# Performance work log

Measured on AMD Instinct MI355X. Metric: run time of the kernel, lower is better.

Reference implementation:

```python
import math
import jax, jax.numpy as jnp
import numpy as np

# ---- DeepSeek-V2-Lite decoder layer config ----
H = 16            # num_attention_heads
D_NOPE = 128      # qk_nope_head_dim
D_ROPE = 64       # qk_rope_head_dim
D_Q = D_NOPE + D_ROPE  # q_head_dim = 192
D_V = 128         # v_head_dim
KV_RANK = 512     # kv_lora_rank
HID = 2048        # hidden_size
INTER = 10944     # intermediate_size (dense MLP)
MAX_POS = 8192
BASE = 10000.0
FACTOR = 40.0     # yarn scaling factor
ORIG_MAX = 4096
BETA_FAST, BETA_SLOW = 32, 1
MSCALE = 0.707
MSCALE_ALL = 0.707
EPS = 1e-6


def _yarn_cos_sin():
    # DeepseekV2LiteYarnRotaryEmbedding._set_cos_sin_cache
    dim = D_ROPE
    ar = np.arange(0, dim, 2, dtype=np.float32) / dim
    freq_extra = 1.0 / BASE ** ar
    freq_inter = 1.0 / (FACTOR * BASE ** ar)

    def corr_dim(num_rot):
        return dim * math.log(ORIG_MAX / (num_rot * 2 * math.pi)) / (2 * math.log(BASE))

    low = max(math.floor(corr_dim(BETA_FAST)), 0)
    high = min(math.ceil(corr_dim(BETA_SLOW)), dim - 1)
    hi = high + 0.001 if low == high else high
    ramp = np.clip((np.arange(dim // 2, dtype=np.float32) - low) / (hi - low), 0.0, 1.0)
    inv_freq_mask = 1.0 - ramp
    inv_freq = freq_inter * (1 - inv_freq_mask) + freq_extra * inv_freq_mask
    t = np.arange(MAX_POS, dtype=np.float32)
    freqs = np.outer(t, inv_freq)

    def get_mscale(s, m):
        return 1.0 if s <= 1 else 0.1 * m * math.log(s) + 1.0

    ms = get_mscale(FACTOR, MSCALE) / get_mscale(FACTOR, MSCALE_ALL)
    emb = np.concatenate([freqs, freqs], axis=-1)
    return jnp.asarray(np.cos(emb) * ms, jnp.float32), jnp.asarray(np.sin(emb) * ms, jnp.float32)

COS_CACHE, SIN_CACHE = _yarn_cos_sin()  # [MAX_POS, D_ROPE]


def _rms(x, w):
    return x * jax.lax.rsqrt(jnp.mean(x * x, axis=-1, keepdims=True) + EPS) * w


def _deinterleave(x):
    # view(..., d//2, 2).transpose(-1, -2).reshape(..., d)
    d = x.shape[-1]
    return x.reshape(x.shape[:-1] + (d // 2, 2)).swapaxes(-1, -2).reshape(x.shape)


def _apply_rope(x, cos, sin):
    x = _deinterleave(x)
    d = x.shape[-1]
    x1, x2 = x[..., : d // 2], x[..., d // 2:]
    return x * cos + jnp.concatenate([-x2, x1], axis=-1) * sin


def _decoder_layer(hidden_states, position_ids, Wq, Wkva, w_kvln, Wkvb, Wo, Wg, Wu, Wd, w_ln1, w_ln2):
    b, s, _ = hidden_states.shape
    dt = hidden_states.dtype

    # ---- attention block ----
    residual = hidden_states
    x = _rms(hidden_states, w_ln1)

    q = (x @ Wq.T).reshape(b, s, H, D_Q)                 # [b,s,h,192]
    q_nope, q_pe = q[..., :D_NOPE], q[..., D_NOPE:]

    ckv = x @ Wkva.T                                     # [b,s,576]
    c, k_pe = ckv[..., :KV_RANK], ckv[..., KV_RANK:][:, :, None, :]  # [b,s,512],[b,s,1,64]
    kv = (_rms(c, w_kvln) @ Wkvb.T).reshape(b, s, H, D_NOPE + D_V)
    k_nope, v = kv[..., :D_NOPE], kv[..., D_NOPE:]

    cos = COS_CACHE[position_ids][:, :, None, :].astype(dt)  # unsqueeze_dim=2
    sin = SIN_CACHE[position_ids][:, :, None, :].astype(dt)
    q_pe = _apply_rope(q_pe, cos, sin)
    k_pe = _apply_rope(k_pe, cos, sin)

    qf = jnp.concatenate([q_nope, q_pe], axis=-1)                          # [b,s,h,192]
    kf = jnp.concatenate([k_nope, jnp.broadcast_to(k_pe, (b, s, H, D_ROPE))], axis=-1)

    scale = D_Q ** -0.5
    scores = jnp.einsum('bqhd,bkhd->bhqk', qf, kf) * scale
    causal = jnp.tril(jnp.ones((s, s), dtype=bool))
    scores = jnp.where(causal, scores, jnp.finfo(scores.dtype).min)
    probs = jax.nn.softmax(scores, axis=-1)
    attn = jnp.einsum('bhqk,bkhd->bqhd', probs, v).reshape(b, s, H * D_V)
    x = residual + attn @ Wo.T

    # ---- MLP block (SwiGLU) ----
    residual = x
    y = _rms(x, w_ln2)
    x = residual + (jax.nn.silu(y @ Wg.T) * (y @ Wu.T)) @ Wd.T
    return x


def setup_inputs() -> dict:
    key = jax.random.key(0)
    ks = jax.random.split(key, 12)
    B, S = 2, 2048
    sd = 0.02
    inp = {
        'hidden_states': jax.random.normal(ks[0], (B, S, HID), jnp.float32),
        'position_ids': jnp.broadcast_to(jnp.arange(S, dtype=jnp.int32), (B, S)),
        'Wq': jax.random.normal(ks[1], (H * D_Q, HID), jnp.float32) * sd,
        'Wkva': jax.random.normal(ks[2], (KV_RANK + D_ROPE, HID), jnp.float32) * sd,
        'w_kvln': jnp.ones((KV_RANK,), jnp.float32),
        'Wkvb': jax.random.normal(ks[3], (H * (D_NOPE + D_V), KV_RANK), jnp.float32) * sd,
        'Wo': jax.random.normal(ks[4], (HID, H * D_V), jnp.float32) * sd,
        'Wg': jax.random.normal(ks[5], (INTER, HID), jnp.float32) * sd,
        'Wu': jax.random.normal(ks[6], (INTER, HID), jnp.float32) * sd,
        'Wd': jax.random.normal(ks[7], (HID, INTER), jnp.float32) * sd,
        'w_ln1': jnp.ones((HID,), jnp.float32),
        'w_ln2': jnp.ones((HID,), jnp.float32),
    }
    return inp


def reference(hidden_states, position_ids, Wq, Wkva, w_kvln, Wkvb, Wo, Wg, Wu, Wd, w_ln1, w_ln2):
    return _decoder_layer(hidden_states, position_ids, Wq, Wkva, w_kvln, Wkvb, Wo, Wg, Wu, Wd, w_ln1, w_ln2)
```

## Files before the change

kernel.cpp:

```cpp
#include <hip/hip_runtime.h>
#include <hip/hip_bf16.h>
#include <math.h>


typedef short short8 __attribute__((ext_vector_type(8)));
typedef short short4v __attribute__((ext_vector_type(4)));
typedef float f32x4 __attribute__((ext_vector_type(4)));

static __device__ __forceinline__ float bf2f(ushort u) {
  union { uint i; float f; } v; v.i = ((uint)u) << 16; return v.f;
}
static __device__ __forceinline__ ushort f2bf(float x) {
  union { float f; uint i; } v; v.f = x;
  uint r = v.i + 0x7fffu + ((v.i >> 16) & 1u);
  return (ushort)(r >> 16);
}

static __device__ __forceinline__ void glds16(const ushort* g, ushort* l) {
  __builtin_amdgcn_global_load_lds(
      (const __attribute__((address_space(1))) unsigned int*)g,
      (__attribute__((address_space(3))) unsigned int*)l, 16, 0, 0);
}

__global__ __launch_bounds__(256)
void cvt_bf16(const float* __restrict__ in, ushort* __restrict__ out, int n8) {
  int i = blockIdx.x * 256 + threadIdx.x;
  if (i >= n8) return;
  float4 a = ((const float4*)in)[2 * i];
  float4 b = ((const float4*)in)[2 * i + 1];
  short8 o;
  o[0] = (short)f2bf(a.x); o[1] = (short)f2bf(a.y);
  o[2] = (short)f2bf(a.z); o[3] = (short)f2bf(a.w);
  o[4] = (short)f2bf(b.x); o[5] = (short)f2bf(b.y);
  o[6] = (short)f2bf(b.z); o[7] = (short)f2bf(b.w);
  ((short8*)out)[i] = o;
}

__global__ __launch_bounds__(256)
void rms_bf16(const float* __restrict__ in, int istride, int width, float inv_w,
              const float* __restrict__ w, ushort* __restrict__ out, int ostride) {
  const int row = blockIdx.x;
  const float* x = in + (size_t)row * istride;
  float ss = 0.f;
  for (int i = threadIdx.x; i < width; i += 256) { float v = x[i]; ss += v * v; }
#pragma unroll
  for (int off = 32; off > 0; off >>= 1) ss += __shfl_xor(ss, off);
  __shared__ float red[4];
  if ((threadIdx.x & 63) == 0) red[threadIdx.x >> 6] = ss;
  __syncthreads();
  float tot = red[0] + red[1] + red[2] + red[3];
  float scale = rsqrtf(tot * inv_w + 1e-6f);
  ushort* o = out + (size_t)row * ostride;
  for (int i = threadIdx.x; i < width; i += 256) o[i] = f2bf(x[i] * scale * w[i]);
}

template<int EPI>
__global__ __launch_bounds__(256, 2)
void gemm_as(const ushort* __restrict__ A, const ushort* __restrict__ B,
             void* __restrict__ Cv, const void* __restrict__ resv,
             int M, int N, int K) {
  __shared__ ushort As[128 * 64];
  __shared__ ushort Bs[128 * 64];
  const int tid = threadIdx.x;
  const int wave = tid >> 6, lane = tid & 63;
  const int m0 = blockIdx.x * 128, n0 = blockIdx.y * 128;
  const int lm = lane & 15, quad = lane >> 4;
  const int wm = (wave & 1) * 64, wn = (wave >> 1) * 64;

  const int lrow = lane >> 3;
  const int lcq  = lane & 7;
  const int gu   = lcq ^ lrow;
  const ushort* gA[4];
  const ushort* gB[4];
  ushort* lA[4];
  ushort* lB[4];
#pragma unroll
  for (int j = 0; j < 4; ++j) {
    const int r = wave * 32 + j * 8 + lrow;
    gA[j] = A + (size_t)(m0 + r) * K + gu * 8;
    int br = n0 + r; if (br > N - 1) br = N - 1;
    gB[j] = B + (size_t)br * K + gu * 8;
    lA[j] = &As[(wave * 32 + j * 8) * 64];
    lB[j] = &Bs[(wave * 32 + j * 8) * 64];
  }

  f32x4 acc[4][4];
  const f32x4 z4 = {0.f, 0.f, 0.f, 0.f};
#pragma unroll
  for (int i = 0; i < 4; ++i)
#pragma unroll
    for (int j = 0; j < 4; ++j) acc[i][j] = z4;

  const int sw = lm & 7;

  for (int k0 = 0; k0 < K; k0 += 64) {
#pragma unroll
    for (int j = 0; j < 4; ++j) glds16(gA[j] + k0, lA[j]);
#pragma unroll
    for (int j = 0; j < 4; ++j) glds16(gB[j] + k0, lB[j]);
    __syncthreads();

#pragma unroll
    for (int kk = 0; kk < 2; ++kk) {
      const int us = ((kk * 4 + quad) ^ sw) * 8;
      short8 afr[4], bfr[4];
#pragma unroll
      for (int mt = 0; mt < 4; ++mt)
        afr[mt] = *(const short8*)&As[(wm + mt * 16 + lm) * 64 + us];
#pragma unroll
      for (int nt = 0; nt < 4; ++nt)
        bfr[nt] = *(const short8*)&Bs[(wn + nt * 16 + lm) * 64 + us];
#pragma unroll
      for (int mt = 0; mt < 4; ++mt)
#pragma unroll
        for (int nt = 0; nt < 4; ++nt)
          acc[mt][nt] = __builtin_amdgcn_mfma_f32_16x16x32_bf16(
              afr[mt], bfr[nt], acc[mt][nt], 0, 0, 0);
    }
    __syncthreads();
  }

#pragma unroll
  for (int mt = 0; mt < 4; ++mt) {
#pragma unroll
    for (int r = 0; r < 4; ++r) {
      const int grow = m0 + wm + mt * 16 + quad * 4 + r;
#pragma unroll
      for (int nt = 0; nt < 4; ++nt) {
        const int gcol = n0 + wn + nt * 16 + lm;
        if (gcol < N) {
          const size_t idx = (size_t)grow * N + gcol;
          float vacc = acc[mt][nt][r];
          if (EPI == 0) {
            ((ushort*)Cv)[idx] = f2bf(vacc);
          } else if (EPI == 1) {
            ((float*)Cv)[idx] = vacc;
          } else if (EPI == 2) {
            ((float*)Cv)[idx] = vacc + ((const float*)resv)[idx];
          } else if (EPI == 3) {
            float gv = bf2f(((const ushort*)resv)[idx]);
            ((ushort*)Cv)[idx] = f2bf(gv / (1.f + __expf(-gv)) * vacc);
          } else {
            if (gcol < 3072)
              ((ushort*)Cv)[(size_t)grow * 3072 + gcol] = f2bf(vacc);
            else
              ((float*)resv)[(size_t)grow * 576 + (gcol - 3072)] = vacc;
          }
        }
      }
    }
  }
}

__global__ __launch_bounds__(64)
void rope_kernel(ushort* __restrict__ q, const float* __restrict__ ckv,
                 const int* __restrict__ pos_ids, ushort* __restrict__ kpe) {
  const int t = blockIdx.x;
  const int j = threadIdx.x;
  const int j2 = j & 31;
  const float ar = (float)j2 * (1.f / 32.f);
  const float fe = exp2f(-ar * 13.287712379549449f);
  const float fi = fe * 0.025f;
  float ramp = ((float)j2 - 10.f) * (1.f / 13.f);
  ramp = fminf(fmaxf(ramp, 0.f), 1.f);
  const float invf = fi * ramp + fe * (1.f - ramp);
  const float ang = (float)pos_ids[t] * invf;
  float s, c;
  __sincosf(ang, &s, &c);
  const bool lo = j < 32;
  {
    const float* kp = ckv + (size_t)t * 576 + 512;
    float x0 = kp[2 * j2], x1 = kp[2 * j2 + 1];
    float o = lo ? (x0 * c - x1 * s) : (x1 * c + x0 * s);
    kpe[(size_t)t * 64 + j] = f2bf(o);
  }
  for (int h = 0; h < 16; ++h) {
    ushort* qp = q + (size_t)t * 3072 + h * 192 + 128;
    float x0 = bf2f(qp[2 * j2]), x1 = bf2f(qp[2 * j2 + 1]);
    float o = lo ? (x0 * c - x1 * s) : (x1 * c + x0 * s);
    __syncthreads();
    qp[j] = f2bf(o);
  }
}

__global__ __launch_bounds__(256, 2)
void attn_mfma(const ushort* __restrict__ q, const ushort* __restrict__ kv,
               const ushort* __restrict__ kpe, ushort* __restrict__ out) {
  const int qt = (int)gridDim.x - 1 - (int)blockIdx.x;
  const int bh = blockIdx.y;
  const int b = bh >> 4, h = bh & 15;
  const int tid = threadIdx.x;
  const int wave = tid >> 6, lane = tid & 63;
  const int lm = lane & 15, quad = lane >> 4;
  const int wq = wave * 32;
  const float scale = 0.07216878364870323f;

  __shared__ __align__(16) char smem[62464];
  ushort (*Ks)[200] = (ushort(*)[200])smem;
  ushort (*Vt)[72]  = (ushort(*)[72])(smem + 25600);
  ushort (*Pm)[72]  = (ushort(*)[72])(smem + 44032);
  ushort (*Qs)[200] = (ushort(*)[200])smem;

  const size_t tok0 = (size_t)b * 2048;
  const int q0 = qt * 128;

  {
    const ushort* qbase = q + (tok0 + q0) * 3072 + (size_t)h * 192;
#pragma unroll
    for (int it = 0; it < 12; ++it) {
      int idx = (it * 256 + tid) * 8;
      int row = idx / 192, col = idx % 192;
      *(uint4*)&Qs[row][col] = *(const uint4*)(qbase + (size_t)row * 3072 + col);
    }
  }
  __syncthreads();
  short8 qf[2][6];
#pragma unroll
  for (int mt = 0; mt < 2; ++mt)
#pragma unroll
    for (int kk = 0; kk < 6; ++kk)
      qf[mt][kk] = *(const short8*)&Qs[wq + mt * 16 + lm][kk * 32 + quad * 8];
  __syncthreads();

  f32x4 o[2][8];
  const f32x4 z4 = {0.f, 0.f, 0.f, 0.f};
#pragma unroll
  for (int mt = 0; mt < 2; ++mt)
#pragma unroll
    for (int nt = 0; nt < 8; ++nt) o[mt][nt] = z4;
  float m_run[8], l_run[8];
#pragma unroll
  for (int i = 0; i < 8; ++i) { m_run[i] = -3.0e38f; l_run[i] = 0.f; }

  const int nkt = 2 * qt + 2;
  for (int kt = 0; kt < nkt; ++kt) {
    const int kb = kt * 64;
    {
      const int krow = tid >> 2, kq = tid & 3;
      const ushort* src = kv + ((tok0 + kb + krow) * 16 + h) * 256 + kq * 32;
#pragma unroll
      for (int i = 0; i < 4; ++i)
        *(uint4*)&Ks[krow][kq * 32 + i * 8] = *(const uint4*)(src + i * 8);
      const ushort* psrc = kpe + (tok0 + kb + krow) * 64 + kq * 16;
      *(uint4*)&Ks[krow][128 + kq * 16]     = *(const uint4*)(psrc);
      *(uint4*)&Ks[krow][128 + kq * 16 + 8] = *(const uint4*)(psrc + 8);
      const int kgrp = (tid & 15) * 4, dgrp = (tid >> 4) * 8;
      uint4 vv[4];
#pragma unroll
      for (int i = 0; i < 4; ++i)
        vv[i] = *(const uint4*)(kv + ((tok0 + kb + kgrp + i) * 16 + h) * 256 + 128 + dgrp);
#pragma unroll
      for (int j = 0; j < 8; ++j) {
        short4v w;
#pragma unroll
        for (int i = 0; i < 4; ++i) w[i] = (short)((const ushort*)&vv[i])[j];
        *(short4v*)&Vt[dgrp + j][kgrp] = w;
      }
    }
    __syncthreads();

    f32x4 s_acc[2][4];
#pragma unroll
    for (int mt = 0; mt < 2; ++mt)
#pragma unroll
      for (int nt = 0; nt < 4; ++nt) s_acc[mt][nt] = z4;
#pragma unroll
    for (int kk = 0; kk < 6; ++kk) {
      short8 kf[4];
#pragma unroll
      for (int nt = 0; nt < 4; ++nt)
        kf[nt] = *(const short8*)&Ks[nt * 16 + lm][kk * 32 + quad * 8];
#pragma unroll
      for (int mt = 0; mt < 2; ++mt)
#pragma unroll
        for (int nt = 0; nt < 4; ++nt)
          s_acc[mt][nt] = __builtin_amdgcn_mfma_f32_16x16x32_bf16(
              qf[mt][kk], kf[nt], s_acc[mt][nt], 0, 0, 0);
    }

    const bool full = (kb + 63) <= (q0 + wq);
#pragma unroll
    for (int mt = 0; mt < 2; ++mt) {
#pragma unroll
      for (int r = 0; r < 4; ++r) {
        const int qg = q0 + wq + mt * 16 + quad * 4 + r;
        float sv[4];
        float rm = -3.0e38f;
        if (full) {
#pragma unroll
          for (int nt = 0; nt < 4; ++nt) {
            float s = s_acc[mt][nt][r] * scale;
            sv[nt] = s;
            rm = fmaxf(rm, s);
          }
        } else {
#pragma unroll
          for (int nt = 0; nt < 4; ++nt) {
            const int key = kb + nt * 16 + lm;
            float s = s_acc[mt][nt][r] * scale;
            s = (key <= qg) ? s : -3.0e38f;
            sv[nt] = s;
            rm = fmaxf(rm, s);
          }
        }
#pragma unroll
        for (int off = 1; off < 16; off <<= 1) rm = fmaxf(rm, __shfl_xor(rm, off));
        const int li = mt * 4 + r;
        const float mnew = fmaxf(m_run[li], rm);
        const float alpha = __expf(m_run[li] - mnew);
        m_run[li] = mnew;
        float rs = 0.f;
        ushort pb[4];
#pragma unroll
        for (int nt = 0; nt < 4; ++nt) {
          float p = __expf(sv[nt] - mnew);
          rs += p;
          pb[nt] = f2bf(p);
        }
#pragma unroll
        for (int off = 1; off < 16; off <<= 1) rs += __shfl_xor(rs, off);
        l_run[li] = l_run[li] * alpha + rs;
#pragma unroll
        for (int nt = 0; nt < 8; ++nt) o[mt][nt][r] *= alpha;
        const int qrow = wq + mt * 16 + quad * 4 + r;
#pragma unroll
        for (int nt = 0; nt < 4; ++nt) Pm[qrow][nt * 16 + lm] = pb[nt];
      }
    }

#pragma unroll
    for (int kt2 = 0; kt2 < 2; ++kt2) {
      short8 pa[2];
#pragma unroll
      for (int mt = 0; mt < 2; ++mt)
        pa[mt] = *(const short8*)&Pm[wq + mt * 16 + lm][kt2 * 32 + quad * 8];
#pragma unroll
      for (int nt = 0; nt < 8; ++nt) {
        short8 vb = *(const short8*)&Vt[nt * 16 + lm][kt2 * 32 + quad * 8];
#pragma unroll
        for (int mt = 0; mt < 2; ++mt)
          o[mt][nt] = __builtin_amdgcn_mfma_f32_16x16x32_bf16(
              pa[mt], vb, o[mt][nt], 0, 0, 0);
      }
    }
    __syncthreads();
  }

  ushort* obase = out + (tok0 + q0) * 2048 + h * 128;
#pragma unroll
  for (int mt = 0; mt < 2; ++mt) {
#pragma unroll
    for (int r = 0; r < 4; ++r) {
      const int qrow = wq + mt * 16 + quad * 4 + r;
      const float inv = 1.f / l_run[mt * 4 + r];
#pragma unroll
      for (int nt = 0; nt < 8; ++nt)
        obase[(size_t)qrow * 2048 + nt * 16 + lm] = f2bf(o[mt][nt][r] * inv);
    }
  }
}

extern "C" void kernel_launch(void* const* d_in, const int* in_sizes, int n_in,
                              void* d_out, int out_size, void* d_ws, size_t ws_size,
                              hipStream_t stream) {
  const float* hidden = (const float*)d_in[0];
  const int*   pos    = (const int*)d_in[1];
  const float* Wq     = (const float*)d_in[2];
  const float* Wkva   = (const float*)d_in[3];
  const float* w_kvln = (const float*)d_in[4];
  const float* Wkvb   = (const float*)d_in[5];
  const float* Wo     = (const float*)d_in[6];
  const float* Wg     = (const float*)d_in[7];
  const float* Wu     = (const float*)d_in[8];
  const float* Wd     = (const float*)d_in[9];
  const float* w_ln1  = (const float*)d_in[10];
  const float* w_ln2  = (const float*)d_in[11];
  float* out = (float*)d_out;

  char* ws = (char*)d_ws;
  ushort* xn    = (ushort*)(ws);
  char*   R1    = ws + 16777216;
  ushort* qb    = (ushort*)(R1);
  float*  ckv   = (float*)(R1 + 25165824);
  ushort* cn    = (ushort*)(R1 + 34603008);
  ushort* kvb   = (ushort*)(R1 + 38797312);
  ushort* kpe   = (ushort*)(R1 + 72351744);
  ushort* attno = (ushort*)(R1 + 72876032);
  ushort* gb    = (ushort*)(R1);
  float*  h1    = (float*)(ws + 196083712);

  char* WSL = ws + 106430464;
  ushort* wq_bf   = (ushort*)(WSL);
  ushort* wkva_bf = (ushort*)(WSL + 12582912);
  ushort* wkvb_bf = (ushort*)(WSL + 14942208);
  ushort* wo_bf   = (ushort*)(WSL + 19136512);
  ushort* wg_bf   = (ushort*)(WSL);
  ushort* wu_bf   = (ushort*)(WSL + 44826624);
  ushort* wd_bf   = (ushort*)(WSL + 44826624);

  cvt_bf16<<<3072, 256, 0, stream>>>(Wq,   wq_bf,   786432);
  cvt_bf16<<<576,  256, 0, stream>>>(Wkva, wkva_bf, 147456);
  cvt_bf16<<<1024, 256, 0, stream>>>(Wkvb, wkvb_bf, 262144);
  cvt_bf16<<<2048, 256, 0, stream>>>(Wo,   wo_bf,   524288);
  cvt_bf16<<<10944, 256, 0, stream>>>(Wu,  wu_bf,   2801664);

  rms_bf16<<<4096, 256, 0, stream>>>(hidden, 2048, 2048, 1.f / 2048.f, w_ln1, xn, 2048);
  gemm_as<4><<<dim3(32, 29), 256, 0, stream>>>(xn, wq_bf, qb, ckv, 4096, 3648, 2048);
  rms_bf16<<<4096, 256, 0, stream>>>(ckv, 576, 512, 1.f / 512.f, w_kvln, cn, 512);
  gemm_as<0><<<dim3(32, 32), 256, 0, stream>>>(cn, wkvb_bf, kvb, nullptr, 4096, 4096, 512);
  rope_kernel<<<4096, 64, 0, stream>>>(qb, ckv, pos, kpe);
  attn_mfma<<<dim3(16, 32), 256, 0, stream>>>(qb, kvb, kpe, attno);
  gemm_as<2><<<dim3(32, 16), 256, 0, stream>>>(attno, wo_bf, h1, hidden, 4096, 2048, 2048);
  rms_bf16<<<4096, 256, 0, stream>>>(h1, 2048, 2048, 1.f / 2048.f, w_ln2, xn, 2048);

  cvt_bf16<<<10944, 256, 0, stream>>>(Wg, wg_bf, 2801664);
  gemm_as<0><<<dim3(32, 86), 256, 0, stream>>>(xn, wg_bf, gb, nullptr, 4096, 10944, 2048);
  gemm_as<3><<<dim3(32, 86), 256, 0, stream>>>(xn, wu_bf, gb, gb, 4096, 10944, 2048);
  cvt_bf16<<<10944, 256, 0, stream>>>(Wd, wd_bf, 2801664);
  gemm_as<2><<<dim3(32, 16), 256, 0, stream>>>(gb, wd_bf, out, h1, 4096, 2048, 10944);
}
```

Measured before the change: 1.325 ms.

## Replace GEMM with 256-wide tiled, 4-stage async-pipelined kernel with XCD remapping

Replaces the 128x128 single-buffered GEMM with a 512-thread kernel using 256x256 or 128x256 tiles and a 4-deep ring of LDS buffers, filled by global_load_lds three K-steps ahead, with vmcnt waits. It adds an XCD-aware workgroup remapping for L2 locality, a new LDS swizzle for 32-wide K slices, and s_setprio around the MFMA bursts. The aim is to hide global load latency and raise data reuse per block. In exchange it uses more LDS and registers (up to 32 accumulators per wave), which may lower occupancy, and with large tiles the smaller GEMMs have fewer blocks than CUs.

```diff
diff --git a/kernel.cpp b/kernel.cpp
--- a/kernel.cpp
+++ b/kernel.cpp
@@ -21,6 +21,8 @@
       (const __attribute__((address_space(1))) unsigned int*)g,
       (__attribute__((address_space(3))) unsigned int*)l, 16, 0, 0);
 }
+
+#define WAITVM(N) asm volatile("s_waitcnt vmcnt(%0)" ::"n"(N) : "memory")
 
 __global__ __launch_bounds__(256)
 void cvt_bf16(const float* __restrict__ in, ushort* __restrict__ out, int n8) {
@@ -54,87 +56,119 @@
   for (int i = threadIdx.x; i < width; i += 256) o[i] = f2bf(x[i] * scale * w[i]);
 }
 
-template<int EPI>
-__global__ __launch_bounds__(256, 2)
-void gemm_as(const ushort* __restrict__ A, const ushort* __restrict__ B,
+template<int EPI, int BMH>
+__global__ __launch_bounds__(512, 2)
+void gemm256(const ushort* __restrict__ A, const ushort* __restrict__ B,
              void* __restrict__ Cv, const void* __restrict__ resv,
              int M, int N, int K) {
-  __shared__ ushort As[128 * 64];
-  __shared__ ushort Bs[128 * 64];
+  constexpr int BM  = BMH * 128;
+  constexpr int MR  = BMH * 4;
+  constexpr int LPT = BMH + 2;
+  __shared__ __align__(16) ushort As[4][BM * 32];
+  __shared__ __align__(16) ushort Bs[4][256 * 32];
   const int tid = threadIdx.x;
   const int wave = tid >> 6, lane = tid & 63;
-  const int m0 = blockIdx.x * 128, n0 = blockIdx.y * 128;
   const int lm = lane & 15, quad = lane >> 4;
-  const int wm = (wave & 1) * 64, wn = (wave >> 1) * 64;
-
-  const int lrow = lane >> 3;
-  const int lcq  = lane & 7;
-  const int gu   = lcq ^ lrow;
-  const ushort* gA[4];
-  const ushort* gB[4];
-  ushort* lA[4];
-  ushort* lB[4];
-#pragma unroll
-  for (int j = 0; j < 4; ++j) {
-    const int r = wave * 32 + j * 8 + lrow;
-    gA[j] = A + (size_t)(m0 + r) * K + gu * 8;
-    int br = n0 + r; if (br > N - 1) br = N - 1;
+
+  const int gx = gridDim.x;
+  int wg = blockIdx.y * gx + blockIdx.x;
+  {
+    const int nwg = gx * (int)gridDim.y;
+    const int q = nwg >> 3, r = nwg & 7;
+    const int xcd = wg & 7, i = wg >> 3;
+    wg = (xcd < r ? xcd * (q + 1) : r * (q + 1) + (xcd - r) * q) + i;
+  }
+  const int m0 = (wg % gx) * BM, n0 = (wg / gx) * 256;
+
+  const int wmg = wave >> 2, wng = wave & 3;
+  const int am = wmg * (BM / 2);
+  const int bn = wng * 64;
+
+  const int srow = lane >> 2;
+  const int gu = (lane & 3) ^ (srow & 3) ^ ((srow >> 2) & 3);
+  const ushort* gA[BMH];
+  ushort* lA[BMH];
+#pragma unroll
+  for (int j = 0; j < BMH; ++j) {
+    const int r = wave * (16 * BMH) + j * 16;
+    gA[j] = A + (size_t)(m0 + r + srow) * K + gu * 8;
+    lA[j] = &As[0][0] + r * 32;
+  }
+  const ushort* gB[2];
+  ushort* lB[2];
+#pragma unroll
+  for (int j = 0; j < 2; ++j) {
+    const int r = wave * 32 + j * 16;
+    int br = n0 + r + srow; if (br > N - 1) br = N - 1;
     gB[j] = B + (size_t)br * K + gu * 8;
-    lA[j] = &As[(wave * 32 + j * 8) * 64];
-    lB[j] = &Bs[(wave * 32 + j * 8) * 64];
-  }
-
-  f32x4 acc[4][4];
+    lB[j] = &Bs[0][0] + r * 32;
+  }
+
+  auto stage = [&](int t) {
+    const int b = t & 3;
+#pragma unroll
+    for (int j = 0; j < BMH; ++j) glds16(gA[j] + t * 32, lA[j] + b * (BM * 32));
+#pragma unroll
+    for (int j = 0; j < 2; ++j)  glds16(gB[j] + t * 32, lB[j] + b * (256 * 32));
+  };
+
+  f32x4 acc[MR][4];
   const f32x4 z4 = {0.f, 0.f, 0.f, 0.f};
 #pragma unroll
-  for (int i = 0; i < 4; ++i)
+  for (int i = 0; i < MR; ++i)
 #pragma unroll
     for (int j = 0; j < 4; ++j) acc[i][j] = z4;
 
-  const int sw = lm & 7;
-
-  for (int k0 = 0; k0 < K; k0 += 64) {
-#pragma unroll
-    for (int j = 0; j < 4; ++j) glds16(gA[j] + k0, lA[j]);
-#pragma unroll
-    for (int j = 0; j < 4; ++j) glds16(gB[j] + k0, lB[j]);
-    __syncthreads();
-
-#pragma unroll
-    for (int kk = 0; kk < 2; ++kk) {
-      const int us = ((kk * 4 + quad) ^ sw) * 8;
-      short8 afr[4], bfr[4];
-#pragma unroll
-      for (int mt = 0; mt < 4; ++mt)
-        afr[mt] = *(const short8*)&As[(wm + mt * 16 + lm) * 64 + us];
-#pragma unroll
-      for (int nt = 0; nt < 4; ++nt)
-        bfr[nt] = *(const short8*)&Bs[(wn + nt * 16 + lm) * 64 + us];
-#pragma unroll
-      for (int mt = 0; mt < 4; ++mt)
-#pragma unroll
-        for (int nt = 0; nt < 4; ++nt)
-          acc[mt][nt] = __builtin_amdgcn_mfma_f32_16x16x32_bf16(
-              afr[mt], bfr[nt], acc[mt][nt], 0, 0, 0);
-    }
-    __syncthreads();
-  }
-
-#pragma unroll
-  for (int mt = 0; mt < 4; ++mt) {
+  const int sw8 = (quad ^ (lm & 3) ^ ((lm >> 2) & 3)) * 8;
+
+  const int nt = K >> 5;
+  stage(0); stage(1); stage(2);
+
+  for (int t = 0; t < nt; ++t) {
+    if (t + 3 < nt) {
+      stage(t + 3);
+      WAITVM(3 * LPT);
+    } else {
+      const int rem = nt - 1 - t;
+      if (rem == 2)      WAITVM(2 * LPT);
+      else if (rem == 1) WAITVM(1 * LPT);
+      else               WAITVM(0);
+    }
+    __builtin_amdgcn_s_barrier();
+
+    const int b = t & 3;
+    short8 af[MR], bf[4];
+#pragma unroll
+    for (int i = 0; i < MR; ++i)
+      af[i] = *(const short8*)&As[b][(am + i * 16 + lm) * 32 + sw8];
+#pragma unroll
+    for (int j = 0; j < 4; ++j)
+      bf[j] = *(const short8*)&Bs[b][(bn + j * 16 + lm) * 32 + sw8];
+
+    __builtin_amdgcn_s_setprio(1);
+#pragma unroll
+    for (int i = 0; i < MR; ++i)
+#pragma unroll
+      for (int j = 0; j < 4; ++j)
+        acc[i][j] = __builtin_amdgcn_mfma_f32_16x16x32_bf16(
+            af[i], bf[j], acc[i][j], 0, 0, 0);
+    __builtin_amdgcn_s_setprio(0);
+    __builtin_amdgcn_s_barrier();
+  }
+
+#pragma unroll
+  for (int i = 0; i < MR; ++i) {
 #pragma unroll
     for (int r = 0; r < 4; ++r) {
-      const int grow = m0 + wm + mt * 16 + quad * 4 + r;
-#pragma unroll
-      for (int nt = 0; nt < 4; ++nt) {
-        const int gcol = n0 + wn + nt * 16 + lm;
+      const int grow = m0 + am + i * 16 + quad * 4 + r;
+#pragma unroll
+      for (int j = 0; j < 4; ++j) {
+        const int gcol = n0 + bn + j * 16 + lm;
         if (gcol < N) {
           const size_t idx = (size_t)grow * N + gcol;
-          float vacc = acc[mt][nt][r];
+          float vacc = acc[i][j][r];
           if (EPI == 0) {
             ((ushort*)Cv)[idx] = f2bf(vacc);
-          } else if (EPI == 1) {
-            ((float*)Cv)[idx] = vacc;
           } else if (EPI == 2) {
             ((float*)Cv)[idx] = vacc + ((const float*)resv)[idx];
           } else if (EPI == 3) {
@@ -405,17 +439,17 @@
   cvt_bf16<<<10944, 256, 0, stream>>>(Wu,  wu_bf,   2801664);
 
   rms_bf16<<<4096, 256, 0, stream>>>(hidden, 2048, 2048, 1.f / 2048.f, w_ln1, xn, 2048);
-  gemm_as<4><<<dim3(32, 29), 256, 0, stream>>>(xn, wq_bf, qb, ckv, 4096, 3648, 2048);
+  gemm256<4, 2><<<dim3(16, 15), 512, 0, stream>>>(xn, wq_bf, qb, ckv, 4096, 3648, 2048);
   rms_bf16<<<4096, 256, 0, stream>>>(ckv, 576, 512, 1.f / 512.f, w_kvln, cn, 512);
-  gemm_as<0><<<dim3(32, 32), 256, 0, stream>>>(cn, wkvb_bf, kvb, nullptr, 4096, 4096, 512);
+  gemm256<0, 2><<<dim3(16, 16), 512, 0, stream>>>(cn, wkvb_bf, kvb, nullptr, 4096, 4096, 512);
   rope_kernel<<<4096, 64, 0, stream>>>(qb, ckv, pos, kpe);
   attn_mfma<<<dim3(16, 32), 256, 0, stream>>>(qb, kvb, kpe, attno);
-  gemm_as<2><<<dim3(32, 16), 256, 0, stream>>>(attno, wo_bf, h1, hidden, 4096, 2048, 2048);
+  gemm256<2, 1><<<dim3(32, 8), 512, 0, stream>>>(attno, wo_bf, h1, hidden, 4096, 2048, 2048);
   rms_bf16<<<4096, 256, 0, stream>>>(h1, 2048, 2048, 1.f / 2048.f, w_ln2, xn, 2048);
 
   cvt_bf16<<<10944, 256, 0, stream>>>(Wg, wg_bf, 2801664);
-  gemm_as<0><<<dim3(32, 86), 256, 0, stream>>>(xn, wg_bf, gb, nullptr, 4096, 10944, 2048);
-  gemm_as<3><<<dim3(32, 86), 256, 0, stream>>>(xn, wu_bf, gb, gb, 4096, 10944, 2048);
+  gemm256<0, 2><<<dim3(16, 43), 512, 0, stream>>>(xn, wg_bf, gb, nullptr, 4096, 10944, 2048);
+  gemm256<3, 2><<<dim3(16, 43), 512, 0, stream>>>(xn, wu_bf, gb, gb, 4096, 10944, 2048);
   cvt_bf16<<<10944, 256, 0, stream>>>(Wd, wd_bf, 2801664);
-  gemm_as<2><<<dim3(32, 16), 256, 0, stream>>>(gb, wd_bf, out, h1, 4096, 2048, 10944);
-}
+  gemm256<2, 1><<<dim3(32, 8), 512, 0, stream>>>(gb, wd_bf, out, h1, 4096, 2048, 10944);
+}
```

Result: slower. 1.667 ms (+25.8%).
